# Kernel optimization log

Measured on AMD Instinct MI355X. Metric: run time of the kernel, lower is better.

## Reference

```python
import jax, jax.numpy as jnp
import numpy as np

D_MODEL = 2048
N_LATENTS = 64
D_LATENT = 1024
N_HEADS = 16
D_H = D_LATENT // N_HEADS


def _split_heads(t):
    B, T, _ = t.shape
    return t.reshape(B, T, N_HEADS, D_H).transpose(0, 2, 1, 3)  # [B,H,T,d_h]


def _merge_heads(t):
    B, H, T, d = t.shape
    return t.transpose(0, 2, 1, 3).reshape(B, T, H * d)


def _attn(Q, K, V):
    scores = jnp.einsum('bhqd,bhkd->bhqk', Q, K) / jnp.sqrt(jnp.asarray(D_H, Q.dtype))
    w = jax.nn.softmax(scores, axis=-1)
    return jnp.einsum('bhqk,bhkd->bhqd', w, V)


def setup_inputs() -> dict:
    key = jax.random.key(0)
    ks = jax.random.split(key, 9)
    s_in = 1.0 / np.sqrt(D_MODEL)
    s_lat = 1.0 / np.sqrt(D_LATENT)
    return {
        'x': jax.random.normal(ks[0], (4, 4096, D_MODEL), dtype=jnp.float32),
        'L': jax.random.normal(ks[1], (N_LATENTS, D_LATENT), dtype=jnp.float32),
        'W_q_lat': jax.random.normal(ks[2], (D_LATENT, D_LATENT), dtype=jnp.float32) * s_lat,
        'W_k_in': jax.random.normal(ks[3], (D_MODEL, D_LATENT), dtype=jnp.float32) * s_in,
        'W_v_in': jax.random.normal(ks[4], (D_MODEL, D_LATENT), dtype=jnp.float32) * s_in,
        'W_q_in': jax.random.normal(ks[5], (D_MODEL, D_LATENT), dtype=jnp.float32) * s_in,
        'W_k_lat': jax.random.normal(ks[6], (D_LATENT, D_LATENT), dtype=jnp.float32) * s_lat,
        'W_v_lat': jax.random.normal(ks[7], (D_LATENT, D_LATENT), dtype=jnp.float32) * s_lat,
        'W_out': jax.random.normal(ks[8], (D_LATENT, D_MODEL), dtype=jnp.float32) * s_lat,
    }


def reference(x, L, W_q_lat, W_k_in, W_v_in, W_q_in, W_k_lat, W_v_lat, W_out):
    B = x.shape[0]
    Lb = jnp.broadcast_to(L[None], (B, N_LATENTS, D_LATENT))
    # Stage 1: latents attend to input tokens (cross-attention)
    Q = _split_heads(Lb @ W_q_lat)
    K = _split_heads(x @ W_k_in)
    V = _split_heads(x @ W_v_in)
    z = _merge_heads(_attn(Q, K, V))  # [B, n_latents, d_latent]
    # Stage 2: latent self-attention
    Ql = _split_heads(z @ W_q_lat)
    Kl = _split_heads(z @ W_k_lat)
    Vl = _split_heads(z @ W_v_lat)
    z2 = _merge_heads(_attn(Ql, Kl, Vl))
    # Stage 3: input tokens attend to latents (cross-attention back)
    Qx = _split_heads(x @ W_q_in)
    Kz = _split_heads(z2 @ W_k_lat)
    Vz = _split_heads(z2 @ W_v_lat)
    x_latent = _merge_heads(_attn(Qx, Kz, Vz))  # [B, N, d_latent]
    return x_latent @ W_out
```

## Files before the change

kernel.cpp:

```cpp
#include <hip/hip_runtime.h>


#define SEQ      4096
#define NHEADS   16
#define SCALE    0.125f

typedef short bfrag __attribute__((ext_vector_type(8)));
typedef float facc  __attribute__((ext_vector_type(4)));

__device__ __forceinline__ unsigned short f2bf(float f) {
  unsigned u = __float_as_uint(f);
  u += 0x7FFFu + ((u >> 16) & 1u);
  return (unsigned short)(u >> 16);
}
__device__ __forceinline__ float bf2f(unsigned short h) {
  return __uint_as_float(((unsigned)h) << 16);
}
__device__ __forceinline__ unsigned pack_hl(float a, float b, unsigned &lo) {
  unsigned short ha = f2bf(a), hb = f2bf(b);
  unsigned short la = f2bf(a - bf2f(ha)), lb = f2bf(b - bf2f(hb));
  lo = (unsigned)la | ((unsigned)lb << 16);
  return (unsigned)ha | ((unsigned)hb << 16);
}
__device__ __forceinline__ void split8(const float* f, bfrag &h, bfrag &l) {
#pragma unroll
  for (int j = 0; j < 8; j++) {
    unsigned short hi = f2bf(f[j]);
    h[j] = (short)hi;
    l[j] = (short)f2bf(f[j] - bf2f(hi));
  }
}

__device__ __forceinline__ void gl_lds16(const void* g, void* l) {
  __builtin_amdgcn_global_load_lds(
      (const __attribute__((address_space(1))) void*)g,
      (__attribute__((address_space(3))) void*)l, 16, 0, 0);
}

__device__ __forceinline__ void write_split16(unsigned short* Hp, unsigned short* Lp,
                                              const float* o, float inv) {
  uint4 H0, H1, L0, L1;
#pragma unroll
  for (int k = 0; k < 8; k++) {
    unsigned lo;
    unsigned hi = pack_hl(o[2*k] * inv, o[2*k+1] * inv, lo);
    if (k < 4) { (&H0.x)[k] = hi; (&L0.x)[k] = lo; }
    else       { (&H1.x)[k-4] = hi; (&L1.x)[k-4] = lo; }
  }
  *(uint4*)Hp       = H0;
  *(uint4*)(Hp + 8) = H1;
  *(uint4*)Lp       = L0;
  *(uint4*)(Lp + 8) = L1;
}

__global__ __launch_bounds__(256) void prep_weight_kernel(
    const float* __restrict__ W, int K, int N,
    unsigned short* __restrict__ Th, unsigned short* __restrict__ Tl)
{
  __shared__ float tile[64][68];
  const int k0 = blockIdx.x * 64, n0 = blockIdx.y * 64;
  const int tid = threadIdx.x;
  const int r = tid >> 2, q = tid & 3;
#pragma unroll
  for (int j = 0; j < 4; j++)
    *(float4*)&tile[r][q*16 + j*4] =
        *(const float4*)&W[(size_t)(k0 + r) * N + n0 + q*16 + j*4];
  __syncthreads();
  const size_t obase = (size_t)(n0 + r) * K + k0 + q*16;
#pragma unroll
  for (int g = 0; g < 2; g++) {
    float f[8];
#pragma unroll
    for (int e = 0; e < 8; e++) f[e] = tile[q*16 + g*8 + e][r];
    uint4 H, Lo;
    H.x = pack_hl(f[0], f[1], Lo.x);
    H.y = pack_hl(f[2], f[3], Lo.y);
    H.z = pack_hl(f[4], f[5], Lo.z);
    H.w = pack_hl(f[6], f[7], Lo.w);
    *(uint4*)&Th[obase + g*8] = H;
    *(uint4*)&Tl[obase + g*8] = Lo;
  }
}

__global__ __launch_bounds__(256) void split_f32_kernel(
    const float* __restrict__ X, unsigned short* __restrict__ H,
    unsigned short* __restrict__ Lo, int n8)
{
  int idx = blockIdx.x * 256 + threadIdx.x;
  if (idx >= n8) return;
  const float4 a = *(const float4*)&X[(size_t)idx*8];
  const float4 b = *(const float4*)&X[(size_t)idx*8 + 4];
  uint4 Hh, Ll;
  Hh.x = pack_hl(a.x, a.y, Ll.x);
  Hh.y = pack_hl(a.z, a.w, Ll.y);
  Hh.z = pack_hl(b.x, b.y, Ll.z);
  Hh.w = pack_hl(b.z, b.w, Ll.w);
  *(uint4*)&H[(size_t)idx*8]  = Hh;
  *(uint4*)&Lo[(size_t)idx*8] = Ll;
}

__global__ __launch_bounds__(256, 2) void gemm_dma_kernel(
    const unsigned short* __restrict__ Ah, const unsigned short* __restrict__ Al,
    const unsigned short* __restrict__ Bh, const unsigned short* __restrict__ Bl,
    float* __restrict__ C, int M, int N, int K)
{
  __shared__ unsigned short sAh[256*32], sAl[256*32], sBh[128*32], sBl[128*32];
  const int tid = threadIdx.x;
  const int m0 = blockIdx.x * 256, n0 = blockIdx.y * 128;
  const int wave = tid >> 6, lane = tid & 63;
  const int lrow = lane & 15, lq = lane >> 4;
  const int wm = (wave & 1) * 128, wn = (wave >> 1) * 64;

  const int srow = lane >> 2, schunk = lane & 3;
  size_t aoff[4], boff[2];
#pragma unroll
  for (int j = 0; j < 4; j++) {
    const int R = 64*wave + 16*j + srow;
    int rg = m0 + R;
    if (rg > M-1) rg = M-1;
    const int c = (schunk - (R >> 1)) & 3;
    aoff[j] = ((size_t)rg * K + c*8) * 2;
  }
#pragma unroll
  for (int j = 0; j < 2; j++) {
    const int R = 32*wave + 16*j + srow;
    const int rg = n0 + R;
    const int c = (schunk - (R >> 1)) & 3;
    boff[j] = ((size_t)rg * K + c*8) * 2;
  }
  const char* Ahc = (const char*)Ah;  const char* Alc = (const char*)Al;
  const char* Bhc = (const char*)Bh;  const char* Blc = (const char*)Bl;

  facc acc[8][4] = {};

  for (int k0 = 0; k0 < K; k0 += 32) {
    const size_t kb = (size_t)k0 * 2;
#pragma unroll
    for (int j = 0; j < 4; j++) {
      gl_lds16(Ahc + aoff[j] + kb, (char*)sAh + (64*wave + 16*j)*64);
      gl_lds16(Alc + aoff[j] + kb, (char*)sAl + (64*wave + 16*j)*64);
    }
#pragma unroll
    for (int j = 0; j < 2; j++) {
      gl_lds16(Bhc + boff[j] + kb, (char*)sBh + (32*wave + 16*j)*64);
      gl_lds16(Blc + boff[j] + kb, (char*)sBl + (32*wave + 16*j)*64);
    }
    __syncthreads();

    bfrag bh[4], bl[4];
#pragma unroll
    for (int ni = 0; ni < 4; ni++) {
      const int R = wn + ni*16 + lrow;
      const int slot = (lq + (R >> 1)) & 3;
      const int bo = R*32 + slot*8;
      bh[ni] = *(const bfrag*)&sBh[bo];
      bl[ni] = *(const bfrag*)&sBl[bo];
    }
#pragma unroll
    for (int mi = 0; mi < 8; mi++) {
      const int R = wm + mi*16 + lrow;
      const int slot = (lq + (R >> 1)) & 3;
      const int ao = R*32 + slot*8;
      const bfrag ah = *(const bfrag*)&sAh[ao];
      const bfrag al = *(const bfrag*)&sAl[ao];
#pragma unroll
      for (int ni = 0; ni < 4; ni++) {
        acc[mi][ni] = __builtin_amdgcn_mfma_f32_16x16x32_bf16(ah, bh[ni], acc[mi][ni], 0, 0, 0);
        acc[mi][ni] = __builtin_amdgcn_mfma_f32_16x16x32_bf16(ah, bl[ni], acc[mi][ni], 0, 0, 0);
        acc[mi][ni] = __builtin_amdgcn_mfma_f32_16x16x32_bf16(al, bh[ni], acc[mi][ni], 0, 0, 0);
      }
    }
    __syncthreads();
  }

#pragma unroll
  for (int mi = 0; mi < 8; mi++) {
#pragma unroll
    for (int r = 0; r < 4; r++) {
      const int row = m0 + wm + mi*16 + lq*4 + r;
      if (row < M) {
        float* Crow = C + (size_t)row * N + n0 + wn + lrow;
#pragma unroll
        for (int ni = 0; ni < 4; ni++)
          Crow[ni*16] = acc[mi][ni][r];
      }
    }
  }
}

__global__ __launch_bounds__(256) void attn1_kernel(
    const float* __restrict__ Qlat,
    const float* __restrict__ KV,
    float* __restrict__ mPart, float* __restrict__ lPart, float* __restrict__ oPart)
{
  __shared__ float Ks[64][68], Vs[64][68], Ps[64][68];
  const int tid = threadIdx.x;
  const int chunk = blockIdx.x, h = blockIdx.y, b = blockIdx.z;
  const int i = tid >> 2, q = tid & 3, db = q * 16, rot = q * 20;

  float4 qreg[16];
#pragma unroll
  for (int dd = 0; dd < 16; dd++) {
    const int c = (4*dd + rot) & 63;
    qreg[dd] = *(const float4*)&Qlat[(size_t)i*1024 + h*64 + c];
  }
  float m_i = -__builtin_inff(), l_i = 0.f;
  float o[16];
#pragma unroll
  for (int dd = 0; dd < 16; dd++) o[dd] = 0.f;

  for (int kt = 0; kt < 8; kt++) {
    const int jg = chunk*512 + kt*64;
    const size_t rb = ((size_t)b*SEQ + jg + i) * 3072;
#pragma unroll
    for (int jj = 0; jj < 4; jj++) {
      *(float4*)&Ks[i][db + jj*4] = *(const float4*)&KV[rb + h*64 + db + jj*4];
      *(float4*)&Vs[i][db + jj*4] = *(const float4*)&KV[rb + 1024 + h*64 + db + jj*4];
    }
    __syncthreads();

    float s[16];
#pragma unroll
    for (int jj = 0; jj < 16; jj++) {
      const int j = db + jj;
      float4 a4 = make_float4(0.f, 0.f, 0.f, 0.f);
#pragma unroll
      for (int dd = 0; dd < 16; dd++) {
        const int c = (4*dd + rot) & 63;
        const float4 kv = *(const float4*)&Ks[j][c];
        a4.x += qreg[dd].x*kv.x; a4.y += qreg[dd].y*kv.y;
        a4.z += qreg[dd].z*kv.z; a4.w += qreg[dd].w*kv.w;
      }
      s[jj] = (a4.x + a4.y + a4.z + a4.w) * SCALE;
    }
    float mt = s[0];
#pragma unroll
    for (int jj = 1; jj < 16; jj++) mt = fmaxf(mt, s[jj]);
    mt = fmaxf(mt, __shfl_xor(mt, 1));
    mt = fmaxf(mt, __shfl_xor(mt, 2));
    const float m_new = fmaxf(m_i, mt);
    const float fac = __expf(m_i - m_new);
    l_i *= fac;
#pragma unroll
    for (int dd = 0; dd < 16; dd++) o[dd] *= fac;
    float ps = 0.f;
#pragma unroll
    for (int jj = 0; jj < 16; jj++) {
      const float p = __expf(s[jj] - m_new);
      Ps[i][db + jj] = p;
      ps += p;
    }
    ps += __shfl_xor(ps, 1);
    ps += __shfl_xor(ps, 2);
    l_i += ps;
    m_i = m_new;
    __syncthreads();
    for (int j = 0; j < 64; j++) {
      const float w = Ps[i][j];
#pragma unroll
      for (int dd = 0; dd < 16; dd += 4) {
        const float4 vv = *(const float4*)&Vs[j][db + dd];
        o[dd+0] += w*vv.x; o[dd+1] += w*vv.y; o[dd+2] += w*vv.z; o[dd+3] += w*vv.w;
      }
    }
    __syncthreads();
  }
  const int bh = b*NHEADS + h;
  const size_t ob = ((size_t)(bh*8 + chunk)*64 + i)*64 + db;
#pragma unroll
  for (int dd = 0; dd < 16; dd++) oPart[ob + dd] = o[dd];
  if (q == 0) {
    mPart[(bh*8 + chunk)*64 + i] = m_i;
    lPart[(bh*8 + chunk)*64 + i] = l_i;
  }
}

__global__ __launch_bounds__(256) void attn1_combine_kernel(
    const float* __restrict__ mPart, const float* __restrict__ lPart,
    const float* __restrict__ oPart,
    unsigned short* __restrict__ Zh, unsigned short* __restrict__ Zl)
{
  const int h = blockIdx.x, b = blockIdx.y;
  const int tid = threadIdx.x;
  const int i = tid >> 2, q = tid & 3, db = q * 16;
  const int bh = b*NHEADS + h;
  float mv[8];
  float M = -__builtin_inff();
#pragma unroll
  for (int c = 0; c < 8; c++) { mv[c] = mPart[(bh*8 + c)*64 + i]; M = fmaxf(M, mv[c]); }
  float Lt = 0.f, w[8];
#pragma unroll
  for (int c = 0; c < 8; c++) { w[c] = __expf(mv[c] - M); Lt += lPart[(bh*8 + c)*64 + i] * w[c]; }
  float o[16];
#pragma unroll
  for (int dd = 0; dd < 16; dd++) o[dd] = 0.f;
#pragma unroll
  for (int c = 0; c < 8; c++) {
    const float* ob = oPart + ((size_t)(bh*8 + c)*64 + i)*64 + db;
#pragma unroll
    for (int dd = 0; dd < 16; dd += 4) {
      const float4 v = *(const float4*)(ob + dd);
      o[dd+0] += w[c]*v.x; o[dd+1] += w[c]*v.y; o[dd+2] += w[c]*v.z; o[dd+3] += w[c]*v.w;
    }
  }
  const float inv = 1.f / Lt;
  const size_t ob2 = ((size_t)b*64 + i)*1024 + h*64 + db;
  write_split16(Zh + ob2, Zl + ob2, o, inv);
}

__global__ __launch_bounds__(256) void attn_small_kernel(
    const float* __restrict__ Qp, int ldq, int qrows_per_b,
    const float* __restrict__ Kp, int ldk,
    const float* __restrict__ Vp, int ldv,
    unsigned short* __restrict__ Oh, unsigned short* __restrict__ Ol, int ldo)
{
  __shared__ float Ks[64][68], Vs[64][68], Ps[64][68];
  const int tid = threadIdx.x;
  const int tt = blockIdx.x, h = blockIdx.y, b = blockIdx.z;
  const int i = tid >> 2, q = tid & 3, db = q * 16, rot = q * 20;
  const size_t qrow = (size_t)b*qrows_per_b + (size_t)tt*64 + i;
  const size_t krow = (size_t)b*64 + i;

  float4 qreg[16];
#pragma unroll
  for (int dd = 0; dd < 16; dd++) {
    const int c = (4*dd + rot) & 63;
    qreg[dd] = *(const float4*)&Qp[qrow*ldq + h*64 + c];
  }
#pragma unroll
  for (int jj = 0; jj < 4; jj++) {
    *(float4*)&Ks[i][db + jj*4] = *(const float4*)&Kp[krow*ldk + h*64 + db + jj*4];
    *(float4*)&Vs[i][db + jj*4] = *(const float4*)&Vp[krow*ldv + h*64 + db + jj*4];
  }
  __syncthreads();

  float s[16];
#pragma unroll
  for (int jj = 0; jj < 16; jj++) {
    const int j = db + jj;
    float4 a4 = make_float4(0.f, 0.f, 0.f, 0.f);
#pragma unroll
    for (int dd = 0; dd < 16; dd++) {
      const int c = (4*dd + rot) & 63;
      const float4 kv = *(const float4*)&Ks[j][c];
      a4.x += qreg[dd].x*kv.x; a4.y += qreg[dd].y*kv.y;
      a4.z += qreg[dd].z*kv.z; a4.w += qreg[dd].w*kv.w;
    }
    s[jj] = (a4.x + a4.y + a4.z + a4.w) * SCALE;
  }
  float m = s[0];
#pragma unroll
  for (int jj = 1; jj < 16; jj++) m = fmaxf(m, s[jj]);
  m = fmaxf(m, __shfl_xor(m, 1));
  m = fmaxf(m, __shfl_xor(m, 2));
  float l = 0.f;
#pragma unroll
  for (int jj = 0; jj < 16; jj++) {
    const float p = __expf(s[jj] - m);
    Ps[i][db + jj] = p;
    l += p;
  }
  l += __shfl_xor(l, 1);
  l += __shfl_xor(l, 2);
  __syncthreads();
  float o[16];
#pragma unroll
  for (int dd = 0; dd < 16; dd++) o[dd] = 0.f;
  for (int j = 0; j < 64; j++) {
    const float w = Ps[i][j];
#pragma unroll
    for (int dd = 0; dd < 16; dd += 4) {
      const float4 vv = *(const float4*)&Vs[j][db + dd];
      o[dd+0] += w*vv.x; o[dd+1] += w*vv.y; o[dd+2] += w*vv.z; o[dd+3] += w*vv.w;
    }
  }
  const float inv = 1.f / l;
  const size_t ob = qrow*ldo + h*64 + db;
  write_split16(Oh + ob, Ol + ob, o, inv);
}

__global__ __launch_bounds__(256) void attn3_mfma_kernel(
    const float* __restrict__ QKV,
    const float* __restrict__ z2kv,
    unsigned short* __restrict__ Oh, unsigned short* __restrict__ Ol)
{
  __shared__ unsigned short Pb[4][16][72];
  const int tid = threadIdx.x;
  const int wave = tid >> 6, lane = tid & 63;
  const int lrow = lane & 15, lq = lane >> 4;
  const int qt = blockIdx.x, h = blockIdx.y, b = blockIdx.z;
  const size_t tok0 = (size_t)b*SEQ + qt*64 + wave*16;

  bfrag qh[2], ql[2];
  {
    const float* qp = QKV + (tok0 + lrow)*3072 + 2048 + h*64 + lq*8;
#pragma unroll
    for (int ks = 0; ks < 2; ks++) {
      float f[8];
      *(float4*)&f[0] = *(const float4*)(qp + ks*32);
      *(float4*)&f[4] = *(const float4*)(qp + ks*32 + 4);
      split8(f, qh[ks], ql[ks]);
    }
  }
  bfrag kh[4][2], kl[4][2];
#pragma unroll
  for (int ni = 0; ni < 4; ni++) {
    const float* kp = z2kv + (size_t)(b*64 + ni*16 + lrow)*2048 + h*64 + lq*8;
#pragma unroll
    for (int ks = 0; ks < 2; ks++) {
      float f[8];
      *(float4*)&f[0] = *(const float4*)(kp + ks*32);
      *(float4*)&f[4] = *(const float4*)(kp + ks*32 + 4);
      split8(f, kh[ni][ks], kl[ni][ks]);
    }
  }
  facc s[4] = {};
#pragma unroll
  for (int ni = 0; ni < 4; ni++)
#pragma unroll
    for (int ks = 0; ks < 2; ks++) {
      s[ni] = __builtin_amdgcn_mfma_f32_16x16x32_bf16(qh[ks], kh[ni][ks], s[ni], 0, 0, 0);
      s[ni] = __builtin_amdgcn_mfma_f32_16x16x32_bf16(qh[ks], kl[ni][ks], s[ni], 0, 0, 0);
      s[ni] = __builtin_amdgcn_mfma_f32_16x16x32_bf16(ql[ks], kh[ni][ks], s[ni], 0, 0, 0);
    }
  float inv[4];
  float p[4][4];
#pragma unroll
  for (int r = 0; r < 4; r++) {
    float mx = fmaxf(fmaxf(s[0][r], s[1][r]), fmaxf(s[2][r], s[3][r])) * SCALE;
    mx = fmaxf(mx, __shfl_xor(mx, 1));
    mx = fmaxf(mx, __shfl_xor(mx, 2));
    mx = fmaxf(mx, __shfl_xor(mx, 4));
    mx = fmaxf(mx, __shfl_xor(mx, 8));
    float sum = 0.f;
#pragma unroll
    for (int ni = 0; ni < 4; ni++) {
      p[ni][r] = __expf(s[ni][r] * SCALE - mx);
      sum += p[ni][r];
    }
    sum += __shfl_xor(sum, 1);
    sum += __shfl_xor(sum, 2);
    sum += __shfl_xor(sum, 4);
    sum += __shfl_xor(sum, 8);
    inv[r] = 1.f / sum;
  }
#pragma unroll
  for (int ni = 0; ni < 4; ni++)
#pragma unroll
    for (int r = 0; r < 4; r++)
      Pb[wave][lq*4 + r][ni*16 + lrow] = f2bf(p[ni][r]);
  __asm__ volatile("s_waitcnt lgkmcnt(0)" ::: "memory");
  bfrag pa[2];
#pragma unroll
  for (int ks = 0; ks < 2; ks++)
    pa[ks] = *(const bfrag*)&Pb[wave][lrow][ks*32 + lq*8];
  facc o[4] = {};
#pragma unroll
  for (int ni = 0; ni < 4; ni++) {
#pragma unroll
    for (int ks = 0; ks < 2; ks++) {
      float f[8];
#pragma unroll
      for (int jj = 0; jj < 8; jj++)
        f[jj] = z2kv[(size_t)(b*64 + ks*32 + lq*8 + jj)*2048 + 1024 + h*64 + ni*16 + lrow];
      bfrag vh, vl;
      split8(f, vh, vl);
      o[ni] = __builtin_amdgcn_mfma_f32_16x16x32_bf16(pa[ks], vh, o[ni], 0, 0, 0);
      o[ni] = __builtin_amdgcn_mfma_f32_16x16x32_bf16(pa[ks], vl, o[ni], 0, 0, 0);
    }
  }
#pragma unroll
  for (int ni = 0; ni < 4; ni++) {
#pragma unroll
    for (int r = 0; r < 4; r++) {
      const float v = o[ni][r] * inv[r];
      const unsigned short hi = f2bf(v);
      const unsigned short lo = f2bf(v - bf2f(hi));
      const size_t idx = (tok0 + lq*4 + r)*1024 + h*64 + ni*16 + lrow;
      Oh[idx] = hi;
      Ol[idx] = lo;
    }
  }
}

extern "C" void kernel_launch(void* const* d_in, const int* in_sizes, int n_in,
                              void* d_out, int out_size, void* d_ws, size_t ws_size,
                              hipStream_t stream)
{
  const float* x      = (const float*)d_in[0];
  const float* L      = (const float*)d_in[1];
  const float* Wq_lat = (const float*)d_in[2];
  const float* Wk_in  = (const float*)d_in[3];
  const float* Wv_in  = (const float*)d_in[4];
  const float* Wq_in  = (const float*)d_in[5];
  const float* Wk_lat = (const float*)d_in[6];
  const float* Wv_lat = (const float*)d_in[7];
  const float* Wout   = (const float*)d_in[8];
  float* out = (float*)d_out;
  (void)in_sizes; (void)n_in; (void)out_size; (void)ws_size;

  char* ws = (char*)d_ws;
  size_t off = 0;
  auto alloc = [&](size_t bytes) -> char* {
    char* p = ws + off; off += (bytes + 255) & ~(size_t)255; return p;
  };
  unsigned short* wtKVQ_h = (unsigned short*)alloc(3072ull*2048*2);
  unsigned short* wtKVQ_l = (unsigned short*)alloc(3072ull*2048*2);
  unsigned short* wtLat_h = (unsigned short*)alloc(3072ull*1024*2);
  unsigned short* wtLat_l = (unsigned short*)alloc(3072ull*1024*2);
  unsigned short* wtOut_h = (unsigned short*)alloc(2048ull*1024*2);
  unsigned short* wtOut_l = (unsigned short*)alloc(2048ull*1024*2);
  unsigned short* xh    = (unsigned short*)alloc(16384ull*2048*2);
  unsigned short* xl    = (unsigned short*)alloc(16384ull*2048*2);
  unsigned short* Lh    = (unsigned short*)alloc(64ull*1024*2);
  unsigned short* Ll    = (unsigned short*)alloc(64ull*1024*2);
  unsigned short* zh    = (unsigned short*)alloc(256ull*1024*2);
  unsigned short* zl    = (unsigned short*)alloc(256ull*1024*2);
  unsigned short* z2h   = (unsigned short*)alloc(256ull*1024*2);
  unsigned short* z2l   = (unsigned short*)alloc(256ull*1024*2);
  float* qlat  = (float*)alloc(64ull*1024*4);
  float* zqkv  = (float*)alloc(256ull*3072*4);
  float* z2kv  = (float*)alloc(256ull*2048*4);
  float* mPart = (float*)alloc(4ull*16*8*64*4);
  float* lPart = (float*)alloc(4ull*16*8*64*4);
  float* oPart = (float*)alloc(4ull*16*8*64*64*4);
  float* qkv   = (float*)alloc(16384ull*3072*4);
  unsigned short* xlat_h = xh;
  unsigned short* xlat_l = xl;

  dim3 blk(256);

  prep_weight_kernel<<<dim3(32, 16), blk, 0, stream>>>(Wk_in, 2048, 1024, wtKVQ_h, wtKVQ_l);
  prep_weight_kernel<<<dim3(32, 16), blk, 0, stream>>>(Wv_in, 2048, 1024, wtKVQ_h + 1024ull*2048, wtKVQ_l + 1024ull*2048);
  prep_weight_kernel<<<dim3(32, 16), blk, 0, stream>>>(Wq_in, 2048, 1024, wtKVQ_h + 2048ull*2048, wtKVQ_l + 2048ull*2048);
  prep_weight_kernel<<<dim3(16, 16), blk, 0, stream>>>(Wq_lat, 1024, 1024, wtLat_h, wtLat_l);
  prep_weight_kernel<<<dim3(16, 16), blk, 0, stream>>>(Wk_lat, 1024, 1024, wtLat_h + 1024ull*1024, wtLat_l + 1024ull*1024);
  prep_weight_kernel<<<dim3(16, 16), blk, 0, stream>>>(Wv_lat, 1024, 1024, wtLat_h + 2048ull*1024, wtLat_l + 2048ull*1024);
  prep_weight_kernel<<<dim3(16, 32), blk, 0, stream>>>(Wout, 1024, 2048, wtOut_h, wtOut_l);
  split_f32_kernel<<<dim3(16384), blk, 0, stream>>>(x, xh, xl, 16384*2048/8);
  split_f32_kernel<<<dim3(32), blk, 0, stream>>>(L, Lh, Ll, 64*1024/8);

  gemm_dma_kernel<<<dim3(1, 8), blk, 0, stream>>>(Lh, Ll, wtLat_h, wtLat_l, qlat, 64, 1024, 1024);
  gemm_dma_kernel<<<dim3(64, 24), blk, 0, stream>>>(xh, xl, wtKVQ_h, wtKVQ_l, qkv, 16384, 3072, 2048);
  attn1_kernel<<<dim3(8, 16, 4), blk, 0, stream>>>(qlat, qkv, mPart, lPart, oPart);
  attn1_combine_kernel<<<dim3(16, 4), blk, 0, stream>>>(mPart, lPart, oPart, zh, zl);
  gemm_dma_kernel<<<dim3(1, 24), blk, 0, stream>>>(zh, zl, wtLat_h, wtLat_l, zqkv, 256, 3072, 1024);
  attn_small_kernel<<<dim3(1, 16, 4), blk, 0, stream>>>(zqkv, 3072, 64, zqkv + 1024, 3072, zqkv + 2048, 3072, z2h, z2l, 1024);
  gemm_dma_kernel<<<dim3(1, 16), blk, 0, stream>>>(z2h, z2l, wtLat_h + 1024ull*1024, wtLat_l + 1024ull*1024, z2kv, 256, 2048, 1024);
  attn3_mfma_kernel<<<dim3(64, 16, 4), blk, 0, stream>>>(qkv, z2kv, xlat_h, xlat_l);
  gemm_dma_kernel<<<dim3(64, 16), blk, 0, stream>>>(xlat_h, xlat_l, wtOut_h, wtOut_l, out, 16384, 2048, 1024);
}
```

Baseline: 1.282 ms.

## Use 32x32 MFMA in GEMM, MFMA attn1, split-bf16 P in attn3

The main GEMM moves from 16x16x32 MFMA tiles to 32x32x16 MFMA tiles with 4x2 wave-level accumulators and a matching epilogue. The stage-1 cross-attention kernel drops its scalar FP32 dot-product loops for bf16 hi/lo split MFMA, staging K and a transposed V in LDS as bf16 pairs. The stage-3 attention now also splits P into hi/lo bf16 and adds an extra MFMA, which favours accuracy over speed. The larger MFMA shape cuts instruction count and LDS fragment reads per FLOP, but the extra V transpose pass and the added syncs in attn1 cost some time back.

```diff
diff --git a/kernel.cpp b/kernel.cpp
--- a/kernel.cpp
+++ b/kernel.cpp
@@ -5,8 +5,9 @@
 #define NHEADS   16
 #define SCALE    0.125f
 
-typedef short bfrag __attribute__((ext_vector_type(8)));
-typedef float facc  __attribute__((ext_vector_type(4)));
+typedef short bfrag  __attribute__((ext_vector_type(8)));
+typedef float facc   __attribute__((ext_vector_type(4)));
+typedef float facc16 __attribute__((ext_vector_type(16)));
 
 __device__ __forceinline__ unsigned short f2bf(float f) {
   unsigned u = __float_as_uint(f);
@@ -108,7 +109,7 @@
   const int tid = threadIdx.x;
   const int m0 = blockIdx.x * 256, n0 = blockIdx.y * 128;
   const int wave = tid >> 6, lane = tid & 63;
-  const int lrow = lane & 15, lq = lane >> 4;
+  const int lrow = lane & 31, lh = lane >> 5;
   const int wm = (wave & 1) * 128, wn = (wave >> 1) * 64;
 
   const int srow = lane >> 2, schunk = lane & 3;
@@ -131,7 +132,7 @@
   const char* Ahc = (const char*)Ah;  const char* Alc = (const char*)Al;
   const char* Bhc = (const char*)Bh;  const char* Blc = (const char*)Bl;
 
-  facc acc[8][4] = {};
+  facc16 acc[4][2] = {};
 
   for (int k0 = 0; k0 < K; k0 += 32) {
     const size_t kb = (size_t)k0 * 2;
@@ -147,42 +148,48 @@
     }
     __syncthreads();
 
-    bfrag bh[4], bl[4];
-#pragma unroll
-    for (int ni = 0; ni < 4; ni++) {
-      const int R = wn + ni*16 + lrow;
-      const int slot = (lq + (R >> 1)) & 3;
-      const int bo = R*32 + slot*8;
-      bh[ni] = *(const bfrag*)&sBh[bo];
-      bl[ni] = *(const bfrag*)&sBl[bo];
-    }
-#pragma unroll
-    for (int mi = 0; mi < 8; mi++) {
-      const int R = wm + mi*16 + lrow;
-      const int slot = (lq + (R >> 1)) & 3;
-      const int ao = R*32 + slot*8;
-      const bfrag ah = *(const bfrag*)&sAh[ao];
-      const bfrag al = *(const bfrag*)&sAl[ao];
-#pragma unroll
-      for (int ni = 0; ni < 4; ni++) {
-        acc[mi][ni] = __builtin_amdgcn_mfma_f32_16x16x32_bf16(ah, bh[ni], acc[mi][ni], 0, 0, 0);
-        acc[mi][ni] = __builtin_amdgcn_mfma_f32_16x16x32_bf16(ah, bl[ni], acc[mi][ni], 0, 0, 0);
-        acc[mi][ni] = __builtin_amdgcn_mfma_f32_16x16x32_bf16(al, bh[ni], acc[mi][ni], 0, 0, 0);
+#pragma unroll
+    for (int ks = 0; ks < 2; ks++) {
+      const int cc = ks*2 + lh;
+      bfrag bh[2], bl[2];
+#pragma unroll
+      for (int ni = 0; ni < 2; ni++) {
+        const int R = wn + ni*32 + lrow;
+        const int slot = (cc + (R >> 1)) & 3;
+        const int bo = R*32 + slot*8;
+        bh[ni] = *(const bfrag*)&sBh[bo];
+        bl[ni] = *(const bfrag*)&sBl[bo];
       }
+#pragma unroll
+      for (int mi = 0; mi < 4; mi++) {
+        const int R = wm + mi*32 + lrow;
+        const int slot = (cc + (R >> 1)) & 3;
+        const int ao = R*32 + slot*8;
+        const bfrag ah = *(const bfrag*)&sAh[ao];
+        const bfrag al = *(const bfrag*)&sAl[ao];
+#pragma unroll
+        for (int ni = 0; ni < 2; ni++) {
+          acc[mi][ni] = __builtin_amdgcn_mfma_f32_32x32x16_bf16(ah, bh[ni], acc[mi][ni], 0, 0, 0);
+          acc[mi][ni] = __builtin_amdgcn_mfma_f32_32x32x16_bf16(ah, bl[ni], acc[mi][ni], 0, 0, 0);
+          acc[mi][ni] = __builtin_amdgcn_mfma_f32_32x32x16_bf16(al, bh[ni], acc[mi][ni], 0, 0, 0);
+        }
+      }
     }
     __syncthreads();
   }
 
 #pragma unroll
-  for (int mi = 0; mi < 8; mi++) {
-#pragma unroll
-    for (int r = 0; r < 4; r++) {
-      const int row = m0 + wm + mi*16 + lq*4 + r;
-      if (row < M) {
-        float* Crow = C + (size_t)row * N + n0 + wn + lrow;
-#pragma unroll
-        for (int ni = 0; ni < 4; ni++)
-          Crow[ni*16] = acc[mi][ni][r];
+  for (int mi = 0; mi < 4; mi++) {
+#pragma unroll
+    for (int g = 0; g < 4; g++) {
+#pragma unroll
+      for (int r = 0; r < 4; r++) {
+        const int row = m0 + wm + mi*32 + g*8 + lh*4 + r;
+        if (row < M) {
+          float* Crow = C + (size_t)row * N + n0 + wn + lrow;
+          Crow[0]  = acc[mi][0][g*4 + r];
+          Crow[32] = acc[mi][1][g*4 + r];
+        }
       }
     }
   }
@@ -193,85 +200,139 @@
     const float* __restrict__ KV,
     float* __restrict__ mPart, float* __restrict__ lPart, float* __restrict__ oPart)
 {
-  __shared__ float Ks[64][68], Vs[64][68], Ps[64][68];
+  __shared__ unsigned short Kh[64][72], Kl[64][72];
+  __shared__ float Vs[64][68];
+  __shared__ unsigned short Vth[64][72], Vtl[64][72];
+  __shared__ unsigned short Pbh[4][16][72], Pbl[4][16][72];
   const int tid = threadIdx.x;
+  const int wave = tid >> 6, lane = tid & 63;
+  const int lrow = lane & 15, lq = lane >> 4;
   const int chunk = blockIdx.x, h = blockIdx.y, b = blockIdx.z;
-  const int i = tid >> 2, q = tid & 3, db = q * 16, rot = q * 20;
-
-  float4 qreg[16];
-#pragma unroll
-  for (int dd = 0; dd < 16; dd++) {
-    const int c = (4*dd + rot) & 63;
-    qreg[dd] = *(const float4*)&Qlat[(size_t)i*1024 + h*64 + c];
-  }
-  float m_i = -__builtin_inff(), l_i = 0.f;
-  float o[16];
-#pragma unroll
-  for (int dd = 0; dd < 16; dd++) o[dd] = 0.f;
+
+  bfrag qh[2], ql[2];
+  {
+    const float* qp = Qlat + (size_t)(wave*16 + lrow)*1024 + h*64 + lq*8;
+#pragma unroll
+    for (int ks = 0; ks < 2; ks++) {
+      float f[8];
+      *(float4*)&f[0] = *(const float4*)(qp + ks*32);
+      *(float4*)&f[4] = *(const float4*)(qp + ks*32 + 4);
+      split8(f, qh[ks], ql[ks]);
+    }
+  }
+  float m_i[4], l_i[4];
+  facc o[4] = {};
+#pragma unroll
+  for (int r = 0; r < 4; r++) { m_i[r] = -__builtin_inff(); l_i[r] = 0.f; }
+
+  const int stok = tid >> 2, sq = (tid & 3) * 16;
+  const int td = tid >> 2, tg = (tid & 3) * 16;
 
   for (int kt = 0; kt < 8; kt++) {
-    const int jg = chunk*512 + kt*64;
-    const size_t rb = ((size_t)b*SEQ + jg + i) * 3072;
-#pragma unroll
-    for (int jj = 0; jj < 4; jj++) {
-      *(float4*)&Ks[i][db + jj*4] = *(const float4*)&KV[rb + h*64 + db + jj*4];
-      *(float4*)&Vs[i][db + jj*4] = *(const float4*)&KV[rb + 1024 + h*64 + db + jj*4];
+    {
+      const size_t rb = ((size_t)b*SEQ + chunk*512 + kt*64 + stok)*3072 + h*64 + sq;
+      float f[16];
+      *(float4*)&f[0]  = *(const float4*)&KV[rb];
+      *(float4*)&f[4]  = *(const float4*)&KV[rb + 4];
+      *(float4*)&f[8]  = *(const float4*)&KV[rb + 8];
+      *(float4*)&f[12] = *(const float4*)&KV[rb + 12];
+      bfrag h0, l0, h1, l1;
+      split8(f, h0, l0);
+      split8(f + 8, h1, l1);
+      *(bfrag*)&Kh[stok][sq]     = h0;
+      *(bfrag*)&Kh[stok][sq + 8] = h1;
+      *(bfrag*)&Kl[stok][sq]     = l0;
+      *(bfrag*)&Kl[stok][sq + 8] = l1;
+      *(float4*)&Vs[stok][sq]      = *(const float4*)&KV[rb + 1024];
+      *(float4*)&Vs[stok][sq + 4]  = *(const float4*)&KV[rb + 1028];
+      *(float4*)&Vs[stok][sq + 8]  = *(const float4*)&KV[rb + 1032];
+      *(float4*)&Vs[stok][sq + 12] = *(const float4*)&KV[rb + 1036];
     }
     __syncthreads();
-
-    float s[16];
-#pragma unroll
-    for (int jj = 0; jj < 16; jj++) {
-      const int j = db + jj;
-      float4 a4 = make_float4(0.f, 0.f, 0.f, 0.f);
-#pragma unroll
-      for (int dd = 0; dd < 16; dd++) {
-        const int c = (4*dd + rot) & 63;
-        const float4 kv = *(const float4*)&Ks[j][c];
-        a4.x += qreg[dd].x*kv.x; a4.y += qreg[dd].y*kv.y;
-        a4.z += qreg[dd].z*kv.z; a4.w += qreg[dd].w*kv.w;
+    {
+      float f[16];
+#pragma unroll
+      for (int u = 0; u < 16; u++) f[u] = Vs[tg + u][td];
+      bfrag h0, l0, h1, l1;
+      split8(f, h0, l0);
+      split8(f + 8, h1, l1);
+      *(bfrag*)&Vth[td][tg]     = h0;
+      *(bfrag*)&Vth[td][tg + 8] = h1;
+      *(bfrag*)&Vtl[td][tg]     = l0;
+      *(bfrag*)&Vtl[td][tg + 8] = l1;
+    }
+    __syncthreads();
+    facc s[4] = {};
+#pragma unroll
+    for (int ni = 0; ni < 4; ni++) {
+#pragma unroll
+      for (int ks = 0; ks < 2; ks++) {
+        const bfrag kbh = *(const bfrag*)&Kh[ni*16 + lrow][ks*32 + lq*8];
+        const bfrag kbl = *(const bfrag*)&Kl[ni*16 + lrow][ks*32 + lq*8];
+        s[ni] = __builtin_amdgcn_mfma_f32_16x16x32_bf16(qh[ks], kbh, s[ni], 0, 0, 0);
+        s[ni] = __builtin_amdgcn_mfma_f32_16x16x32_bf16(qh[ks], kbl, s[ni], 0, 0, 0);
+        s[ni] = __builtin_amdgcn_mfma_f32_16x16x32_bf16(ql[ks], kbh, s[ni], 0, 0, 0);
       }
-      s[jj] = (a4.x + a4.y + a4.z + a4.w) * SCALE;
-    }
-    float mt = s[0];
-#pragma unroll
-    for (int jj = 1; jj < 16; jj++) mt = fmaxf(mt, s[jj]);
-    mt = fmaxf(mt, __shfl_xor(mt, 1));
-    mt = fmaxf(mt, __shfl_xor(mt, 2));
-    const float m_new = fmaxf(m_i, mt);
-    const float fac = __expf(m_i - m_new);
-    l_i *= fac;
-#pragma unroll
-    for (int dd = 0; dd < 16; dd++) o[dd] *= fac;
-    float ps = 0.f;
-#pragma unroll
-    for (int jj = 0; jj < 16; jj++) {
-      const float p = __expf(s[jj] - m_new);
-      Ps[i][db + jj] = p;
-      ps += p;
-    }
-    ps += __shfl_xor(ps, 1);
-    ps += __shfl_xor(ps, 2);
-    l_i += ps;
-    m_i = m_new;
+    }
+#pragma unroll
+    for (int r = 0; r < 4; r++) {
+      float mx = fmaxf(fmaxf(s[0][r], s[1][r]), fmaxf(s[2][r], s[3][r])) * SCALE;
+      mx = fmaxf(mx, __shfl_xor(mx, 1));
+      mx = fmaxf(mx, __shfl_xor(mx, 2));
+      mx = fmaxf(mx, __shfl_xor(mx, 4));
+      mx = fmaxf(mx, __shfl_xor(mx, 8));
+      const float m_new = fmaxf(m_i[r], mx);
+      const float fac = __expf(m_i[r] - m_new);
+      m_i[r] = m_new;
+      float sum = 0.f;
+#pragma unroll
+      for (int ni = 0; ni < 4; ni++) {
+        const float p = __expf(s[ni][r] * SCALE - m_new);
+        sum += p;
+        const unsigned short ph = f2bf(p);
+        Pbh[wave][lq*4 + r][ni*16 + lrow] = ph;
+        Pbl[wave][lq*4 + r][ni*16 + lrow] = f2bf(p - bf2f(ph));
+      }
+      sum += __shfl_xor(sum, 1);
+      sum += __shfl_xor(sum, 2);
+      sum += __shfl_xor(sum, 4);
+      sum += __shfl_xor(sum, 8);
+      l_i[r] = l_i[r] * fac + sum;
+#pragma unroll
+      for (int nd = 0; nd < 4; nd++) o[nd][r] *= fac;
+    }
+    __asm__ volatile("s_waitcnt lgkmcnt(0)" ::: "memory");
+    bfrag pah[2], pal[2];
+#pragma unroll
+    for (int ks = 0; ks < 2; ks++) {
+      pah[ks] = *(const bfrag*)&Pbh[wave][lrow][ks*32 + lq*8];
+      pal[ks] = *(const bfrag*)&Pbl[wave][lrow][ks*32 + lq*8];
+    }
+#pragma unroll
+    for (int nd = 0; nd < 4; nd++) {
+#pragma unroll
+      for (int ks = 0; ks < 2; ks++) {
+        const bfrag vbh = *(const bfrag*)&Vth[nd*16 + lrow][ks*32 + lq*8];
+        const bfrag vbl = *(const bfrag*)&Vtl[nd*16 + lrow][ks*32 + lq*8];
+        o[nd] = __builtin_amdgcn_mfma_f32_16x16x32_bf16(pah[ks], vbh, o[nd], 0, 0, 0);
+        o[nd] = __builtin_amdgcn_mfma_f32_16x16x32_bf16(pal[ks], vbh, o[nd], 0, 0, 0);
+        o[nd] = __builtin_amdgcn_mfma_f32_16x16x32_bf16(pah[ks], vbl, o[nd], 0, 0, 0);
+      }
+    }
     __syncthreads();
-    for (int j = 0; j < 64; j++) {
-      const float w = Ps[i][j];
-#pragma unroll
-      for (int dd = 0; dd < 16; dd += 4) {
-        const float4 vv = *(const float4*)&Vs[j][db + dd];
-        o[dd+0] += w*vv.x; o[dd+1] += w*vv.y; o[dd+2] += w*vv.z; o[dd+3] += w*vv.w;
-      }
-    }
-    __syncthreads();
   }
   const int bh = b*NHEADS + h;
-  const size_t ob = ((size_t)(bh*8 + chunk)*64 + i)*64 + db;
-#pragma unroll
-  for (int dd = 0; dd < 16; dd++) oPart[ob + dd] = o[dd];
-  if (q == 0) {
-    mPart[(bh*8 + chunk)*64 + i] = m_i;
-    lPart[(bh*8 + chunk)*64 + i] = l_i;
+  const int lat0 = wave*16 + lq*4;
+#pragma unroll
+  for (int r = 0; r < 4; r++) {
+    const size_t ob = ((size_t)(bh*8 + chunk)*64 + lat0 + r)*64;
+#pragma unroll
+    for (int nd = 0; nd < 4; nd++)
+      oPart[ob + nd*16 + lrow] = o[nd][r];
+    if (lrow == 0) {
+      mPart[(bh*8 + chunk)*64 + lat0 + r] = m_i[r];
+      lPart[(bh*8 + chunk)*64 + lat0 + r] = l_i[r];
+    }
   }
 }
 
@@ -384,7 +445,7 @@
     const float* __restrict__ z2kv,
     unsigned short* __restrict__ Oh, unsigned short* __restrict__ Ol)
 {
-  __shared__ unsigned short Pb[4][16][72];
+  __shared__ unsigned short Pbh[4][16][72], Pbl[4][16][72];
   const int tid = threadIdx.x;
   const int wave = tid >> 6, lane = tid & 63;
   const int lrow = lane & 15, lq = lane >> 4;
@@ -424,7 +485,6 @@
       s[ni] = __builtin_amdgcn_mfma_f32_16x16x32_bf16(ql[ks], kh[ni][ks], s[ni], 0, 0, 0);
     }
   float inv[4];
-  float p[4][4];
 #pragma unroll
   for (int r = 0; r < 4; r++) {
     float mx = fmaxf(fmaxf(s[0][r], s[1][r]), fmaxf(s[2][r], s[3][r])) * SCALE;
@@ -435,8 +495,11 @@
     float sum = 0.f;
 #pragma unroll
     for (int ni = 0; ni < 4; ni++) {
-      p[ni][r] = __expf(s[ni][r] * SCALE - mx);
-      sum += p[ni][r];
+      const float p = __expf(s[ni][r] * SCALE - mx);
+      sum += p;
+      const unsigned short ph = f2bf(p);
+      Pbh[wave][lq*4 + r][ni*16 + lrow] = ph;
+      Pbl[wave][lq*4 + r][ni*16 + lrow] = f2bf(p - bf2f(ph));
     }
     sum += __shfl_xor(sum, 1);
     sum += __shfl_xor(sum, 2);
@@ -444,16 +507,13 @@
     sum += __shfl_xor(sum, 8);
     inv[r] = 1.f / sum;
   }
-#pragma unroll
-  for (int ni = 0; ni < 4; ni++)
-#pragma unroll
-    for (int r = 0; r < 4; r++)
-      Pb[wave][lq*4 + r][ni*16 + lrow] = f2bf(p[ni][r]);
   __asm__ volatile("s_waitcnt lgkmcnt(0)" ::: "memory");
-  bfrag pa[2];
-#pragma unroll
-  for (int ks = 0; ks < 2; ks++)
-    pa[ks] = *(const bfrag*)&Pb[wave][lrow][ks*32 + lq*8];
+  bfrag pah[2], pal[2];
+#pragma unroll
+  for (int ks = 0; ks < 2; ks++) {
+    pah[ks] = *(const bfrag*)&Pbh[wave][lrow][ks*32 + lq*8];
+    pal[ks] = *(const bfrag*)&Pbl[wave][lrow][ks*32 + lq*8];
+  }
   facc o[4] = {};
 #pragma unroll
   for (int ni = 0; ni < 4; ni++) {
@@ -465,8 +525,9 @@
         f[jj] = z2kv[(size_t)(b*64 + ks*32 + lq*8 + jj)*2048 + 1024 + h*64 + ni*16 + lrow];
       bfrag vh, vl;
       split8(f, vh, vl);
-      o[ni] = __builtin_amdgcn_mfma_f32_16x16x32_bf16(pa[ks], vh, o[ni], 0, 0, 0);
-      o[ni] = __builtin_amdgcn_mfma_f32_16x16x32_bf16(pa[ks], vl, o[ni], 0, 0, 0);
+      o[ni] = __builtin_amdgcn_mfma_f32_16x16x32_bf16(pah[ks], vh, o[ni], 0, 0, 0);
+      o[ni] = __builtin_amdgcn_mfma_f32_16x16x32_bf16(pal[ks], vh, o[ni], 0, 0, 0);
+      o[ni] = __builtin_amdgcn_mfma_f32_16x16x32_bf16(pah[ks], vl, o[ni], 0, 0, 0);
     }
   }
 #pragma unroll
```

Result: slower. 1.322 ms (+3.1%).
